# Kernel tuning notes

Measured on AMD Instinct MI355X. Metric: run time of the kernel, lower is better.

The kernel has to match this reference:

```python
import jax, jax.numpy as jnp
import numpy as np

T, B, I, N, C = 2048, 512, 28, 256, 2
TAU = 2.0

def _lin_init(key, out_f, in_f):
    # torch nn.Linear default: U(-1/sqrt(in_f), 1/sqrt(in_f)) for weight and bias
    s = 1.0 / np.sqrt(in_f)
    kw, kb = jax.random.split(key)
    W = jax.random.uniform(kw, (out_f, in_f), jnp.float32, -s, s)
    b = jax.random.uniform(kb, (out_f,), jnp.float32, -s, s)
    return W, b

def setup_inputs() -> dict:
    key = jax.random.key(0)
    ks = jax.random.split(key, 8)
    data = jax.random.normal(ks[0], (T, B, I), jnp.float32)
    hier_signal = jax.random.normal(ks[1], (B, N), jnp.float32)
    h0 = 0.1 * jax.random.uniform(ks[2], (B, N), jnp.float32)  # matches 0.1*torch.rand init
    W_in, b_in = _lin_init(ks[3], N, I)   # input_layers[0]
    W_hh, b_hh = _lin_init(ks[4], N, N)   # w_hh[0]
    W_ff, b_ff = _lin_init(ks[5], N, N)   # w_ff_in
    W_fc, b_fc = _lin_init(ks[6], C, N)   # fc[0]
    return dict(data=data, hier_signal=hier_signal, h0=h0,
                W_in=W_in, b_in=b_in, W_hh=W_hh, b_hh=b_hh,
                W_ff=W_ff, b_ff=b_ff, W_fc=W_fc, b_fc=b_fc)

def reference(data, hier_signal, h0, W_in, b_in, W_hh, b_hh, W_ff, b_ff, W_fc, b_fc):
    # recurrent weight has its diagonal zeroed every forward call
    W_hh_z = W_hh * (1.0 - jnp.eye(W_hh.shape[0], dtype=W_hh.dtype))
    # input projection for all timesteps at once: [T,B,N]
    x = jnp.einsum('tbi,ni->tbn', data, W_in) + b_in
    # hierarchical feed-forward signal, constant over time: [B,N]
    ff = hier_signal @ W_ff.T + b_ff
    inv_tau = 1.0 / TAU
    keep = 1.0 - inv_tau

    def step(h, x_t):
        h = jax.nn.leaky_relu(keep * h + (h @ W_hh_z.T + b_hh + ff + x_t) * inv_tau)
        return h, None

    hT, _ = jax.lax.scan(step, h0, x)
    out = hT @ W_fc.T + b_fc  # readout head 0: [B, C]
    return out
```

## Files before the change

### kernel.cpp

```cpp
#include <hip/hip_runtime.h>
#include <stdint.h>
#include <stddef.h>

#define TSTEPS 2048
#define BATCH  512
#define IDIM   28
#define NDIM   256

typedef __attribute__((ext_vector_type(4))) float f32x4;
typedef __attribute__((ext_vector_type(8))) short short8;

#define MFMA __builtin_amdgcn_mfma_f32_16x16x32_bf16

__device__ __forceinline__ short8 pack2(f32x4 a, f32x4 b) {
  union { uint32_t u[4]; short8 s; } r;
  asm("v_cvt_pk_bf16_f32 %0, %1, %2" : "=v"(r.u[0]) : "v"(a[0]), "v"(a[1]));
  asm("v_cvt_pk_bf16_f32 %0, %1, %2" : "=v"(r.u[1]) : "v"(a[2]), "v"(a[3]));
  asm("v_cvt_pk_bf16_f32 %0, %1, %2" : "=v"(r.u[2]) : "v"(b[0]), "v"(b[1]));
  asm("v_cvt_pk_bf16_f32 %0, %1, %2" : "=v"(r.u[3]) : "v"(b[2]), "v"(b[3]));
  return r.s;
}

#define LDS_BARRIER()                                       \
  do {                                                      \
    __asm__ volatile("s_waitcnt lgkmcnt(0)" ::: "memory");  \
    __builtin_amdgcn_s_barrier();                           \
    __asm__ volatile("" ::: "memory");                      \
  } while (0)

#define RNN_STEP(P, DLO, DHI, PF)                                             \
  {                                                                           \
    const short8* rb = (const short8*)(&ldsf[(P)][0][0][0]);                  \
    short8 Bf1 = rb[rd1], Bf4 = rb[rd4], Bf2 = rb[rd2], Bf5 = rb[rd5];        \
    short8 Bf3 = rb[rd3], Bf6 = rb[rd6], Bf7 = rb[rd7];                       \
    short8 Bx = pack2(DLO, DHI);                                              \
    if (PF) {                                                                 \
      DLO = *(const f32x4*)dpf;                                               \
      DHI = *(const f32x4*)(dpf + hiOff);                                     \
      dpf += BATCH * IDIM;                                                    \
    }                                                                         \
    f32x4 aA0, aA1, aB0, aB1;                                                 \
    _Pragma("unroll")                                                         \
    for (int r = 0; r < 4; ++r) {                                             \
      aA0[r] = __builtin_fmaf(0.5f, hc0[r], cst0[r]);                         \
      aA1[r] = __builtin_fmaf(0.5f, hc1[r], cst1[r]);                         \
    }                                                                         \
    f32x4 z4 = {0.f, 0.f, 0.f, 0.f};                                          \
                      \
    aA0 = MFMA(A_hh[0][0], Bown, aA0, 0, 0, 0);                               \
    aA1 = MFMA(A_hh[1][0], Bown, aA1, 0, 0, 0);                               \
    aB0 = MFMA(A_in[0], Bx, z4, 0, 0, 0);                                     \
    aB1 = MFMA(A_in[1], Bx, z4, 0, 0, 0);                                     \
                         \
    aA0 = MFMA(A_hh[0][1], Bf1, aA0, 0, 0, 0);                                \
    aA1 = MFMA(A_hh[1][1], Bf1, aA1, 0, 0, 0);                                \
    aB0 = MFMA(A_hh[0][4], Bf4, aB0, 0, 0, 0);                                \
    aB1 = MFMA(A_hh[1][4], Bf4, aB1, 0, 0, 0);                                \
    aA0 = MFMA(A_hh[0][2], Bf2, aA0, 0, 0, 0);                                \
    aA1 = MFMA(A_hh[1][2], Bf2, aA1, 0, 0, 0);                                \
    aB0 = MFMA(A_hh[0][5], Bf5, aB0, 0, 0, 0);                                \
    aB1 = MFMA(A_hh[1][5], Bf5, aB1, 0, 0, 0);                                \
    aA0 = MFMA(A_hh[0][3], Bf3, aA0, 0, 0, 0);                                \
    aA1 = MFMA(A_hh[1][3], Bf3, aA1, 0, 0, 0);                                \
    aB0 = MFMA(A_hh[0][6], Bf6, aB0, 0, 0, 0);                                \
    aB1 = MFMA(A_hh[1][6], Bf6, aB1, 0, 0, 0);                                \
    aB0 = MFMA(A_hh[0][7], Bf7, aB0, 0, 0, 0);                                \
    aB1 = MFMA(A_hh[1][7], Bf7, aB1, 0, 0, 0);                                \
    _Pragma("unroll")                                                         \
    for (int r = 0; r < 4; ++r) {                                             \
      float p0 = aA0[r] + aB0[r]; hc0[r] = __builtin_fmaxf(p0, 0.01f * p0);   \
      float p1 = aA1[r] + aB1[r]; hc1[r] = __builtin_fmaxf(p1, 0.01f * p1);   \
    }                                                                         \
    Bown = pack2(hc0, hc1);                                                   \
    ((short8*)(&ldsf[(P) ^ 1][0][0][0]))[wr] = Bown;                          \
    LDS_BARRIER();                                                            \
  }

__global__ __launch_bounds__(512, 2)
void rnn_fused(const float* __restrict__ data,
               const float* __restrict__ hier,
               const float* __restrict__ h0,
               const float* __restrict__ W_in,
               const float* __restrict__ b_in,
               const float* __restrict__ W_hh,
               const float* __restrict__ b_hh,
               const float* __restrict__ W_ff,
               const float* __restrict__ b_ff,
               const float* __restrict__ W_fc,
               const float* __restrict__ b_fc,
               float* __restrict__ out)
{
  __shared__ __attribute__((aligned(16))) short ldsf[2][8][64][8];
  __shared__ float ldsh[16][264];

  const int tid  = threadIdx.x;
  const int wave = tid >> 6;
  const int lane = tid & 63;
  const int g    = lane >> 4;
  const int c    = lane & 15;
  const int b0   = blockIdx.x * 16;

  const int m0 = 32 * wave + c;
  const int m1 = m0 + 16;

  const int wr  = wave * 64 + lane;
  const int rd1 = ((wave + 1) & 7) * 64 + lane;
  const int rd2 = ((wave + 2) & 7) * 64 + lane;
  const int rd3 = ((wave + 3) & 7) * 64 + lane;
  const int rd4 = ((wave + 4) & 7) * 64 + lane;
  const int rd5 = ((wave + 5) & 7) * 64 + lane;
  const int rd6 = ((wave + 6) & 7) * 64 + lane;
  const int rd7 = ((wave + 7) & 7) * 64 + lane;

  f32x4 cst0 = {0.f,0.f,0.f,0.f}, cst1 = {0.f,0.f,0.f,0.f};
  {
    const float* hp = hier + (size_t)(b0 + c) * NDIM + 4 * g;
    const float* w0 = W_ff + (size_t)m0 * NDIM + 4 * g;
    const float* w1 = W_ff + (size_t)m1 * NDIM + 4 * g;
#pragma unroll
    for (int kt = 0; kt < 8; ++kt) {
      short8 bh  = pack2(*(const f32x4*)(hp + kt * 32), *(const f32x4*)(hp + kt * 32 + 16));
      short8 af0 = pack2(*(const f32x4*)(w0 + kt * 32), *(const f32x4*)(w0 + kt * 32 + 16));
      short8 af1 = pack2(*(const f32x4*)(w1 + kt * 32), *(const f32x4*)(w1 + kt * 32 + 16));
      cst0 = MFMA(af0, bh, cst0, 0, 0, 0);
      cst1 = MFMA(af1, bh, cst1, 0, 0, 0);
    }
  }
#pragma unroll
  for (int r = 0; r < 4; ++r) {
    const int n0 = 32 * wave + 4 * g + r;
    cst0[r] = 0.5f * (cst0[r] + b_hh[n0]      + b_in[n0]      + b_ff[n0]);
    cst1[r] = 0.5f * (cst1[r] + b_hh[n0 + 16] + b_in[n0 + 16] + b_ff[n0 + 16]);
  }

  short8 A_hh[2][8];
  short8 A_in[2];
#pragma unroll
  for (int i = 0; i < 2; ++i) {
    const int row = 32 * wave + 16 * i + c;
    const float* wrow = W_hh + (size_t)row * NDIM;
#pragma unroll
    for (int j = 0; j < 8; ++j) {
      const int ktg = (wave + j) & 7;
      f32x4 lo = *(const f32x4*)(wrow + 32 * ktg + 4 * g);
      f32x4 hi = *(const f32x4*)(wrow + 32 * ktg + 16 + 4 * g);
#pragma unroll
      for (int q = 0; q < 4; ++q) {
        const int kl = 32 * ktg + 4 * g + q, kh = kl + 16;
        lo[q] = (kl == row) ? 0.f : 0.5f * lo[q];
        hi[q] = (kh == row) ? 0.f : 0.5f * hi[q];
      }
      A_hh[i][j] = pack2(lo, hi);
    }
    const float* p = W_in + (size_t)row * IDIM;
    f32x4 lo = *(const f32x4*)(p + 4 * g);
    f32x4 hi = {0.f, 0.f, 0.f, 0.f};
    if (g < 3) hi = *(const f32x4*)(p + 16 + 4 * g);
#pragma unroll
    for (int q = 0; q < 4; ++q) { lo[q] *= 0.5f; hi[q] *= 0.5f; }
    A_in[i] = pack2(lo, hi);
  }

  f32x4 hc0, hc1;
  short8 Bown;
  {
    const float* hp = h0 + (size_t)(b0 + c) * NDIM + 32 * wave + 4 * g;
    hc0 = *(const f32x4*)(hp + 0);
    hc1 = *(const f32x4*)(hp + 16);
    Bown = pack2(hc0, hc1);
    ((short8*)(&ldsf[0][0][0][0]))[wr] = Bown;
  }

  const int hiOff = (g < 3) ? 16 : -4;
  const float* dpf = data + (size_t)(b0 + c) * IDIM + 4 * g;
  f32x4 dlo0, dlo1, dlo2, dlo3, dhi0, dhi1, dhi2, dhi3;
  dlo0 = *(const f32x4*)dpf; dhi0 = *(const f32x4*)(dpf + hiOff); dpf += BATCH * IDIM;
  dlo1 = *(const f32x4*)dpf; dhi1 = *(const f32x4*)(dpf + hiOff); dpf += BATCH * IDIM;
  dlo2 = *(const f32x4*)dpf; dhi2 = *(const f32x4*)(dpf + hiOff); dpf += BATCH * IDIM;
  dlo3 = *(const f32x4*)dpf; dhi3 = *(const f32x4*)(dpf + hiOff); dpf += BATCH * IDIM;

  __syncthreads();

  for (int t = 0; t < TSTEPS - 4; t += 4) {
    RNN_STEP(0, dlo0, dhi0, 1)
    RNN_STEP(1, dlo1, dhi1, 1)
    RNN_STEP(0, dlo2, dhi2, 1)
    RNN_STEP(1, dlo3, dhi3, 1)
  }
  RNN_STEP(0, dlo0, dhi0, 0)
  RNN_STEP(1, dlo1, dhi1, 0)
  RNN_STEP(0, dlo2, dhi2, 0)
  RNN_STEP(1, dlo3, dhi3, 0)

  *(f32x4*)(&ldsh[c][32 * wave + 4 * g])      = hc0;
  *(f32x4*)(&ldsh[c][32 * wave + 16 + 4 * g]) = hc1;
  __syncthreads();
  if (tid < 32) {
    int b = tid >> 1, cls = tid & 1;
    float s = b_fc[cls];
    const float* wf = W_fc + (size_t)cls * NDIM;
#pragma unroll 8
    for (int n = 0; n < NDIM; ++n) s += ldsh[b][n] * wf[n];
    out[(size_t)(b0 + b) * 2 + cls] = s;
  }
}

extern "C" void kernel_launch(void* const* d_in, const int* in_sizes, int n_in,
                              void* d_out, int out_size, void* d_ws, size_t ws_size,
                              hipStream_t stream) {
  const float* data = (const float*)d_in[0];
  const float* hier = (const float*)d_in[1];
  const float* h0   = (const float*)d_in[2];
  const float* W_in = (const float*)d_in[3];
  const float* b_in = (const float*)d_in[4];
  const float* W_hh = (const float*)d_in[5];
  const float* b_hh = (const float*)d_in[6];
  const float* W_ff = (const float*)d_in[7];
  const float* b_ff = (const float*)d_in[8];
  const float* W_fc = (const float*)d_in[9];
  const float* b_fc = (const float*)d_in[10];
  rnn_fused<<<dim3(BATCH / 16), dim3(512), 0, stream>>>(
      data, hier, h0, W_in, b_in, W_hh, b_hh, W_ff, b_ff, W_fc, b_fc,
      (float*)d_out);
}
```

Baseline: 920.4 us.

## Process two independent 16-row batch groups per block to interleave recurrences

Each block now handles 32 batch rows as two independent 16-row groups, A and B, with separate hidden states and LDS buffers. Both groups' step work runs between one barrier per timestep, so group B's MFMAs can fill the latency of group A's dependency chain. The grid halves from 32 to 16 blocks, leaving most of the 256 CUs idle while per-block register pressure rises. The data prefetch depth drops from four timesteps to one, and the old s_waitcnt-based barrier is replaced by __syncthreads.

```diff
diff --git a/kernel.cpp b/kernel.cpp
--- a/kernel.cpp
+++ b/kernel.cpp
@@ -21,36 +21,22 @@
   return r.s;
 }
 
-#define LDS_BARRIER()                                       \
-  do {                                                      \
-    __asm__ volatile("s_waitcnt lgkmcnt(0)" ::: "memory");  \
-    __builtin_amdgcn_s_barrier();                           \
-    __asm__ volatile("" ::: "memory");                      \
-  } while (0)
-
-#define RNN_STEP(P, DLO, DHI, PF)                                             \
+#define GROUP_STEP(RB, HC0, HC1, CST0, CST1, BOWN, BX, WB)                    \
   {                                                                           \
-    const short8* rb = (const short8*)(&ldsf[(P)][0][0][0]);                  \
-    short8 Bf1 = rb[rd1], Bf4 = rb[rd4], Bf2 = rb[rd2], Bf5 = rb[rd5];        \
-    short8 Bf3 = rb[rd3], Bf6 = rb[rd6], Bf7 = rb[rd7];                       \
-    short8 Bx = pack2(DLO, DHI);                                              \
-    if (PF) {                                                                 \
-      DLO = *(const f32x4*)dpf;                                               \
-      DHI = *(const f32x4*)(dpf + hiOff);                                     \
-      dpf += BATCH * IDIM;                                                    \
-    }                                                                         \
+    short8 Bf1 = RB[rd1], Bf4 = RB[rd4], Bf2 = RB[rd2], Bf5 = RB[rd5];        \
+    short8 Bf3 = RB[rd3], Bf6 = RB[rd6], Bf7 = RB[rd7];                       \
     f32x4 aA0, aA1, aB0, aB1;                                                 \
     _Pragma("unroll")                                                         \
     for (int r = 0; r < 4; ++r) {                                             \
-      aA0[r] = __builtin_fmaf(0.5f, hc0[r], cst0[r]);                         \
-      aA1[r] = __builtin_fmaf(0.5f, hc1[r], cst1[r]);                         \
+      aA0[r] = __builtin_fmaf(0.5f, HC0[r], CST0[r]);                         \
+      aA1[r] = __builtin_fmaf(0.5f, HC1[r], CST1[r]);                         \
     }                                                                         \
     f32x4 z4 = {0.f, 0.f, 0.f, 0.f};                                          \
                       \
-    aA0 = MFMA(A_hh[0][0], Bown, aA0, 0, 0, 0);                               \
-    aA1 = MFMA(A_hh[1][0], Bown, aA1, 0, 0, 0);                               \
-    aB0 = MFMA(A_in[0], Bx, z4, 0, 0, 0);                                     \
-    aB1 = MFMA(A_in[1], Bx, z4, 0, 0, 0);                                     \
+    aA0 = MFMA(A_hh[0][0], BOWN, aA0, 0, 0, 0);                               \
+    aA1 = MFMA(A_hh[1][0], BOWN, aA1, 0, 0, 0);                               \
+    aB0 = MFMA(A_in[0], BX, z4, 0, 0, 0);                                     \
+    aB1 = MFMA(A_in[1], BX, z4, 0, 0, 0);                                     \
                          \
     aA0 = MFMA(A_hh[0][1], Bf1, aA0, 0, 0, 0);                                \
     aA1 = MFMA(A_hh[1][1], Bf1, aA1, 0, 0, 0);                                \
@@ -68,12 +54,33 @@
     aB1 = MFMA(A_hh[1][7], Bf7, aB1, 0, 0, 0);                                \
     _Pragma("unroll")                                                         \
     for (int r = 0; r < 4; ++r) {                                             \
-      float p0 = aA0[r] + aB0[r]; hc0[r] = __builtin_fmaxf(p0, 0.01f * p0);   \
-      float p1 = aA1[r] + aB1[r]; hc1[r] = __builtin_fmaxf(p1, 0.01f * p1);   \
-    }                                                                         \
-    Bown = pack2(hc0, hc1);                                                   \
-    ((short8*)(&ldsf[(P) ^ 1][0][0][0]))[wr] = Bown;                          \
-    LDS_BARRIER();                                                            \
+      float p0 = aA0[r] + aB0[r]; HC0[r] = __builtin_fmaxf(p0, 0.01f * p0);   \
+      float p1 = aA1[r] + aB1[r]; HC1[r] = __builtin_fmaxf(p1, 0.01f * p1);   \
+    }                                                                         \
+    BOWN = pack2(HC0, HC1);                                                   \
+    WB[wr] = BOWN;                                                            \
+  }
+
+#define RNN_PHASE(P, PF)                                                      \
+  {                                                                           \
+    const short8* rbA = (const short8*)(&ldsf[(P)][0][0][0][0]);              \
+    short8* wbA = (short8*)(&ldsf[(P) ^ 1][0][0][0][0]);                      \
+    short8 BxA = pack2(dloA, dhiA);                                           \
+    if (PF) {                                                                 \
+      dloA = *(const f32x4*)dpf;                                              \
+      dhiA = *(const f32x4*)(dpf + hiOff);                                    \
+    }                                                                         \
+    GROUP_STEP(rbA, hcA0, hcA1, cstA0, cstA1, BownA, BxA, wbA)                \
+    const short8* rbB = (const short8*)(&ldsf[(P)][1][0][0][0]);              \
+    short8* wbB = (short8*)(&ldsf[(P) ^ 1][1][0][0][0]);                      \
+    short8 BxB = pack2(dloB, dhiB);                                           \
+    if (PF) {                                                                 \
+      dloB = *(const f32x4*)(dpf + 16 * IDIM);                                \
+      dhiB = *(const f32x4*)(dpf + 16 * IDIM + hiOff);                        \
+      dpf += BATCH * IDIM;                                                    \
+    }                                                                         \
+    GROUP_STEP(rbB, hcB0, hcB1, cstB0, cstB1, BownB, BxB, wbB)                \
+    __syncthreads();                                                          \
   }
 
 __global__ __launch_bounds__(512, 2)
@@ -90,15 +97,15 @@
                const float* __restrict__ b_fc,
                float* __restrict__ out)
 {
-  __shared__ __attribute__((aligned(16))) short ldsf[2][8][64][8];
-  __shared__ float ldsh[16][264];
+  __shared__ __attribute__((aligned(16))) short ldsf[2][2][8][64][8];
+  __shared__ float ldsh[32][264];
 
   const int tid  = threadIdx.x;
   const int wave = tid >> 6;
   const int lane = tid & 63;
   const int g    = lane >> 4;
   const int c    = lane & 15;
-  const int b0   = blockIdx.x * 16;
+  const int b0   = blockIdx.x * 32;
 
   const int m0 = 32 * wave + c;
   const int m1 = m0 + 16;
@@ -112,25 +119,34 @@
   const int rd6 = ((wave + 6) & 7) * 64 + lane;
   const int rd7 = ((wave + 7) & 7) * 64 + lane;
 
-  f32x4 cst0 = {0.f,0.f,0.f,0.f}, cst1 = {0.f,0.f,0.f,0.f};
+  f32x4 cstA0 = {0.f,0.f,0.f,0.f}, cstA1 = {0.f,0.f,0.f,0.f};
+  f32x4 cstB0 = {0.f,0.f,0.f,0.f}, cstB1 = {0.f,0.f,0.f,0.f};
   {
-    const float* hp = hier + (size_t)(b0 + c) * NDIM + 4 * g;
+    const float* hpA = hier + (size_t)(b0 + c) * NDIM + 4 * g;
+    const float* hpB = hpA + 16 * NDIM;
     const float* w0 = W_ff + (size_t)m0 * NDIM + 4 * g;
     const float* w1 = W_ff + (size_t)m1 * NDIM + 4 * g;
 #pragma unroll
     for (int kt = 0; kt < 8; ++kt) {
-      short8 bh  = pack2(*(const f32x4*)(hp + kt * 32), *(const f32x4*)(hp + kt * 32 + 16));
+      short8 bhA = pack2(*(const f32x4*)(hpA + kt * 32), *(const f32x4*)(hpA + kt * 32 + 16));
+      short8 bhB = pack2(*(const f32x4*)(hpB + kt * 32), *(const f32x4*)(hpB + kt * 32 + 16));
       short8 af0 = pack2(*(const f32x4*)(w0 + kt * 32), *(const f32x4*)(w0 + kt * 32 + 16));
       short8 af1 = pack2(*(const f32x4*)(w1 + kt * 32), *(const f32x4*)(w1 + kt * 32 + 16));
-      cst0 = MFMA(af0, bh, cst0, 0, 0, 0);
-      cst1 = MFMA(af1, bh, cst1, 0, 0, 0);
+      cstA0 = MFMA(af0, bhA, cstA0, 0, 0, 0);
+      cstA1 = MFMA(af1, bhA, cstA1, 0, 0, 0);
+      cstB0 = MFMA(af0, bhB, cstB0, 0, 0, 0);
+      cstB1 = MFMA(af1, bhB, cstB1, 0, 0, 0);
     }
   }
 #pragma unroll
   for (int r = 0; r < 4; ++r) {
     const int n0 = 32 * wave + 4 * g + r;
-    cst0[r] = 0.5f * (cst0[r] + b_hh[n0]      + b_in[n0]      + b_ff[n0]);
-    cst1[r] = 0.5f * (cst1[r] + b_hh[n0 + 16] + b_in[n0 + 16] + b_ff[n0 + 16]);
+    const float bs0 = b_hh[n0]      + b_in[n0]      + b_ff[n0];
+    const float bs1 = b_hh[n0 + 16] + b_in[n0 + 16] + b_ff[n0 + 16];
+    cstA0[r] = 0.5f * (cstA0[r] + bs0);
+    cstA1[r] = 0.5f * (cstA1[r] + bs1);
+    cstB0[r] = 0.5f * (cstB0[r] + bs0);
+    cstB1[r] = 0.5f * (cstB1[r] + bs1);
   }
 
   short8 A_hh[2][8];
@@ -161,41 +177,45 @@
     A_in[i] = pack2(lo, hi);
   }
 
-  f32x4 hc0, hc1;
-  short8 Bown;
+  f32x4 hcA0, hcA1, hcB0, hcB1;
+  short8 BownA, BownB;
   {
-    const float* hp = h0 + (size_t)(b0 + c) * NDIM + 32 * wave + 4 * g;
-    hc0 = *(const f32x4*)(hp + 0);
-    hc1 = *(const f32x4*)(hp + 16);
-    Bown = pack2(hc0, hc1);
-    ((short8*)(&ldsf[0][0][0][0]))[wr] = Bown;
+    const float* hpA = h0 + (size_t)(b0 + c) * NDIM + 32 * wave + 4 * g;
+    const float* hpB = hpA + 16 * NDIM;
+    hcA0 = *(const f32x4*)(hpA + 0);
+    hcA1 = *(const f32x4*)(hpA + 16);
+    hcB0 = *(const f32x4*)(hpB + 0);
+    hcB1 = *(const f32x4*)(hpB + 16);
+    BownA = pack2(hcA0, hcA1);
+    BownB = pack2(hcB0, hcB1);
+    ((short8*)(&ldsf[0][0][0][0][0]))[wr] = BownA;
+    ((short8*)(&ldsf[0][1][0][0][0]))[wr] = BownB;
   }
 
   const int hiOff = (g < 3) ? 16 : -4;
   const float* dpf = data + (size_t)(b0 + c) * IDIM + 4 * g;
-  f32x4 dlo0, dlo1, dlo2, dlo3, dhi0, dhi1, dhi2, dhi3;
-  dlo0 = *(const f32x4*)dpf; dhi0 = *(const f32x4*)(dpf + hiOff); dpf += BATCH * IDIM;
-  dlo1 = *(const f32x4*)dpf; dhi1 = *(const f32x4*)(dpf + hiOff); dpf += BATCH * IDIM;
-  dlo2 = *(const f32x4*)dpf; dhi2 = *(const f32x4*)(dpf + hiOff); dpf += BATCH * IDIM;
-  dlo3 = *(const f32x4*)dpf; dhi3 = *(const f32x4*)(dpf + hiOff); dpf += BATCH * IDIM;
+  f32x4 dloA, dhiA, dloB, dhiB;
+  dloA = *(const f32x4*)dpf;
+  dhiA = *(const f32x4*)(dpf + hiOff);
+  dloB = *(const f32x4*)(dpf + 16 * IDIM);
+  dhiB = *(const f32x4*)(dpf + 16 * IDIM + hiOff);
+  dpf += BATCH * IDIM;
 
   __syncthreads();
 
-  for (int t = 0; t < TSTEPS - 4; t += 4) {
-    RNN_STEP(0, dlo0, dhi0, 1)
-    RNN_STEP(1, dlo1, dhi1, 1)
-    RNN_STEP(0, dlo2, dhi2, 1)
-    RNN_STEP(1, dlo3, dhi3, 1)
-  }
-  RNN_STEP(0, dlo0, dhi0, 0)
-  RNN_STEP(1, dlo1, dhi1, 0)
-  RNN_STEP(0, dlo2, dhi2, 0)
-  RNN_STEP(1, dlo3, dhi3, 0)
-
-  *(f32x4*)(&ldsh[c][32 * wave + 4 * g])      = hc0;
-  *(f32x4*)(&ldsh[c][32 * wave + 16 + 4 * g]) = hc1;
+  for (int t = 0; t < TSTEPS - 2; t += 2) {
+    RNN_PHASE(0, 1)
+    RNN_PHASE(1, 1)
+  }
+  RNN_PHASE(0, 1)
+  RNN_PHASE(1, 0)
+
+  *(f32x4*)(&ldsh[c][32 * wave + 4 * g])           = hcA0;
+  *(f32x4*)(&ldsh[c][32 * wave + 16 + 4 * g])      = hcA1;
+  *(f32x4*)(&ldsh[16 + c][32 * wave + 4 * g])      = hcB0;
+  *(f32x4*)(&ldsh[16 + c][32 * wave + 16 + 4 * g]) = hcB1;
   __syncthreads();
-  if (tid < 32) {
+  if (tid < 64) {
     int b = tid >> 1, cls = tid & 1;
     float s = b_fc[cls];
     const float* wf = W_fc + (size_t)cls * NDIM;
@@ -219,7 +239,7 @@
   const float* b_ff = (const float*)d_in[8];
   const float* W_fc = (const float*)d_in[9];
   const float* b_fc = (const float*)d_in[10];
-  rnn_fused<<<dim3(BATCH / 16), dim3(512), 0, stream>>>(
+  rnn_fused<<<dim3(BATCH / 32), dim3(512), 0, stream>>>(
       data, hier, h0, W_in, b_in, W_hh, b_hh, W_ff, b_ff, W_fc, b_fc,
       (float*)d_out);
 }
```

New measurement: 2.168 ms. 2.36x slower.
